# Optimization experiments

Measured on AMD Instinct MI355X. Metric: run time of the kernel, lower is better.

The kernel has to match this reference:

```python
import jax, jax.numpy as jnp
import numpy as np

N_NODES, N_EDGES, CH, FEAT = 20000, 320000, 256, 118


def setup_inputs() -> dict:
    key = jax.random.key(0)
    ks = jax.random.split(key, 8)
    x = jax.random.uniform(ks[0], (N_NODES, FEAT), dtype=jnp.float32)
    edge_index = jax.random.randint(ks[1], (2, N_EDGES), 0, N_NODES, dtype=jnp.int64)
    s = 0.05
    W_embed = jax.random.normal(ks[2], (FEAT, CH), dtype=jnp.float32) * s
    b_embed = jnp.zeros((CH,), jnp.float32)
    W1 = jax.random.normal(ks[3], (CH, CH), dtype=jnp.float32) * s
    b1 = jnp.zeros((CH,), jnp.float32)
    W2 = jax.random.normal(ks[4], (CH, CH), dtype=jnp.float32) * s
    b2 = jnp.zeros((CH,), jnp.float32)
    return {"x": x, "edge_index": edge_index, "W_embed": W_embed, "b_embed": b_embed,
            "W1": W1, "b1": b1, "W2": W2, "b2": b2}


def reference(x, edge_index, W_embed, b_embed, W1, b1, W2, b2):
    n = x.shape[0]
    # node embedding: Linear(118 -> C)
    h = x @ W_embed + b_embed  # [N, C]
    src, dst = edge_index[0], edge_index[1]
    # message: gather x_j per edge, dense1 + exact GELU (dropout = identity in eval)
    msg = jax.nn.gelu(h[src] @ W1 + b1, approximate=False)  # [E, C]
    # mean aggregation into destination nodes
    agg = jax.ops.segment_sum(msg, dst, num_segments=n)  # [N, C]
    cnt = jax.ops.segment_sum(jnp.ones((msg.shape[0],), msg.dtype), dst, num_segments=n)
    agg = agg / jnp.maximum(cnt, 1.0)[:, None]
    # update: dense2 + exact GELU
    out = jax.nn.gelu(agg @ W2 + b2, approximate=False)  # [N, C]
    # final mean over channel dim
    return out.mean(axis=1)  # [N]
```

## Files before the change

kernel.cpp:

```cpp
#include <hip/hip_runtime.h>
#include <math.h>

#define N_NODES 20000
#define N_EDGES 320000
#define CH      256
#define FEAT    118
#define CAP     48

typedef float    f32x4 __attribute__((ext_vector_type(4)));
typedef short    s16x8 __attribute__((ext_vector_type(8)));
typedef _Float16 f16x4 __attribute__((ext_vector_type(4)));
typedef unsigned short u16;

union Frag { s16x8 v; u16 u[8]; };

__device__ __forceinline__ float gelu_exact(float x) {
    return 0.5f * x * (1.0f + erff(x * 0.70710678118654752f));
}
__device__ __forceinline__ u16 f2bf(float f) {
    unsigned u = __float_as_uint(f);
    u = (u + 0x7FFFu + ((u >> 16) & 1u)) >> 16;
    return (u16)u;
}
__device__ __forceinline__ float bf2f(u16 h) { return __uint_as_float(((unsigned)h) << 16); }

__global__ __launch_bounds__(256) void prep(const float* __restrict__ x,
                                            const int* __restrict__ ei,
                                            const float* __restrict__ We,
                                            const float* __restrict__ be,
                                            const float* __restrict__ W1,
                                            const float* __restrict__ b1,
                                            const float* __restrict__ W2,
                                            u16* __restrict__ xh, u16* __restrict__ xl,
                                            int* __restrict__ cnt, int* __restrict__ bins,
                                            u16* __restrict__ w2h, u16* __restrict__ w2l,
                                            u16* __restrict__ wch, u16* __restrict__ wcl,
                                            float* __restrict__ bc) {
    const int b = blockIdx.x, tid = threadIdx.x;
    if (b < 1250) {
        int fid = b * 256 + tid;
        int lane = fid & 63, ks = (fid >> 6) & 3, mt = fid >> 8;
        int row = mt * 16 + (lane & 15);
        int k0 = ks * 32 + (lane >> 4) * 8;
        Frag hi, lo;
        #pragma unroll
        for (int j = 0; j < 8; j++) {
            int k = k0 + j;
            float v = (k < FEAT) ? x[(size_t)row * FEAT + k] : 0.0f;
            u16 h = f2bf(v);
            hi.u[j] = h; lo.u[j] = f2bf(v - bf2f(h));
        }
        ((s16x8*)xh)[fid] = hi.v;
        ((s16x8*)xl)[fid] = lo.v;
    } else if (b < 2500) {
        int e = (b - 1250) * 256 + tid;
        int s = ei[e];
        int d = ei[N_EDGES + e];
        int p = atomicAdd(&cnt[d], 1);
        if (p < CAP) bins[(size_t)d * CAP + p] = s;
    } else if (b < 2532) {
        int fid = (b - 2500) * 256 + tid;
        int lane = fid & 63, ks = (fid >> 6) & 7, nt = fid >> 9;
        int n = nt * 16 + (lane & 15);
        int k0 = ks * 32 + (lane >> 4) * 8;
        Frag hi, lo;
        #pragma unroll
        for (int j = 0; j < 8; j++) {
            float v = W2[(size_t)(k0 + j) * 256 + n];
            u16 h = f2bf(v);
            hi.u[j] = h; lo.u[j] = f2bf(v - bf2f(h));
        }
        ((s16x8*)w2h)[fid] = hi.v;
        ((s16x8*)w2l)[fid] = lo.v;
    } else {
        int f = b - 2532;
        int n = tid;
        if (f < 128) {
            float acc = 0.0f;
            if (f < FEAT) {
                const float* wr = We + (size_t)f * 256;
                #pragma unroll 8
                for (int c = 0; c < 256; c++) acc += wr[c] * W1[(size_t)c * 256 + n];
            }
            int nt = n >> 4, lm = n & 15, ks = f >> 5, q = (f >> 3) & 3, j = f & 7;
            size_t idx = (((size_t)nt * 4 + ks) * 64 + q * 16 + lm) * 8 + j;
            u16 h = f2bf(acc);
            wch[idx] = h;
            wcl[idx] = f2bf(acc - bf2f(h));
        } else {
            float acc = b1[n];
            #pragma unroll 8
            for (int c = 0; c < 256; c++) acc += be[c] * W1[(size_t)c * 256 + n];
            bc[n] = acc;
        }
    }
}

__global__ __launch_bounds__(256) void gemm_main(const u16* __restrict__ Ah_, const u16* __restrict__ Al_,
                                                 const u16* __restrict__ Bh_, const u16* __restrict__ Bl_,
                                                 const float* __restrict__ bias,
                                                 _Float16* __restrict__ Mout) {
    __shared__ _Float16 Ls[32][256];
    const int tid = threadIdx.x, wave = tid >> 6, lane = tid & 63;
    const int quad = lane >> 4, lm = lane & 15;
    const int mt0 = blockIdx.x * 2, nt0 = wave * 4;
    const s16x8* Ah = (const s16x8*)Ah_; const s16x8* Al = (const s16x8*)Al_;
    const s16x8* Bh = (const s16x8*)Bh_; const s16x8* Bl = (const s16x8*)Bl_;
    f32x4 acc[2][4];
    #pragma unroll
    for (int mi = 0; mi < 2; mi++)
        #pragma unroll
        for (int t = 0; t < 4; t++) acc[mi][t] = f32x4{0.f, 0.f, 0.f, 0.f};
    #pragma unroll
    for (int ks = 0; ks < 4; ks++) {
        s16x8 a0h = Ah[((size_t)(mt0 + 0) * 4 + ks) * 64 + lane];
        s16x8 a0l = Al[((size_t)(mt0 + 0) * 4 + ks) * 64 + lane];
        s16x8 a1h = Ah[((size_t)(mt0 + 1) * 4 + ks) * 64 + lane];
        s16x8 a1l = Al[((size_t)(mt0 + 1) * 4 + ks) * 64 + lane];
        #pragma unroll
        for (int t = 0; t < 4; t++) {
            s16x8 bh = Bh[((size_t)(nt0 + t) * 4 + ks) * 64 + lane];
            s16x8 bl = Bl[((size_t)(nt0 + t) * 4 + ks) * 64 + lane];
            acc[0][t] = __builtin_amdgcn_mfma_f32_16x16x32_bf16(a0h, bh, acc[0][t], 0, 0, 0);
            acc[0][t] = __builtin_amdgcn_mfma_f32_16x16x32_bf16(a0l, bh, acc[0][t], 0, 0, 0);
            acc[0][t] = __builtin_amdgcn_mfma_f32_16x16x32_bf16(a0h, bl, acc[0][t], 0, 0, 0);
            acc[1][t] = __builtin_amdgcn_mfma_f32_16x16x32_bf16(a1h, bh, acc[1][t], 0, 0, 0);
            acc[1][t] = __builtin_amdgcn_mfma_f32_16x16x32_bf16(a1l, bh, acc[1][t], 0, 0, 0);
            acc[1][t] = __builtin_amdgcn_mfma_f32_16x16x32_bf16(a1h, bl, acc[1][t], 0, 0, 0);
        }
    }
    #pragma unroll
    for (int t = 0; t < 4; t++) {
        float bn = bias[(nt0 + t) * 16 + lm];
        #pragma unroll
        for (int mi = 0; mi < 2; mi++)
            #pragma unroll
            for (int r = 0; r < 4; r++)
                Ls[mi * 16 + quad * 4 + r][(nt0 + t) * 16 + lm] =
                    (_Float16)gelu_exact(acc[mi][t][r] + bn);
    }
    __syncthreads();
    s16x8* dst = (s16x8*)Mout + (size_t)blockIdx.x * 1024;
    const s16x8* src = (const s16x8*)&Ls[0][0];
    #pragma unroll
    for (int it = 0; it < 4; it++)
        dst[it * 256 + tid] = src[it * 256 + tid];
}

#define LP 272
__global__ __launch_bounds__(256) void agg_mean(const _Float16* __restrict__ M,
                                                const int* __restrict__ cnt,
                                                const int* __restrict__ bins,
                                                const u16* __restrict__ Bh_, const u16* __restrict__ Bl_,
                                                const float* __restrict__ bias,
                                                float* __restrict__ out) {
    __shared__ u16 Lh[32][LP];
    __shared__ u16 Ll[32][LP];
    __shared__ float part[4][32];
    const int tid = threadIdx.x, wave = tid >> 6, lane = tid & 63;
    const int quad = lane >> 4, lm = lane & 15;

    {
        int nb = blockIdx.x * 32 + wave * 8;
        int cfull[8], cc[8], myid[8];
        #pragma unroll
        for (int i = 0; i < 8; i++) {
            cfull[i] = cnt[nb + i];
            cc[i] = min(cfull[i], CAP);
            myid[i] = (lane < CAP) ? bins[(size_t)(nb + i) * CAP + lane] : 0;
        }
        float acc[8][4];
        #pragma unroll
        for (int i = 0; i < 8; i++)
            #pragma unroll
            for (int q = 0; q < 4; q++) acc[i][q] = 0.0f;
        int mx = 0;
        #pragma unroll
        for (int i = 0; i < 8; i++) mx = max(mx, cc[i]);
        for (int j = 0; j < mx; j++) {
            #pragma unroll
            for (int i = 0; i < 8; i++) {
                if (j < cc[i]) {
                    int s = __shfl(myid[i], j, 64);
                    f16x4 v = *(const f16x4*)(M + (size_t)s * CH + lane * 4);
                    acc[i][0] += (float)v.x; acc[i][1] += (float)v.y;
                    acc[i][2] += (float)v.z; acc[i][3] += (float)v.w;
                }
            }
        }
        #pragma unroll
        for (int i = 0; i < 8; i++) {
            float inv = 1.0f / (float)max(cfull[i], 1);
            int row = wave * 8 + i;
            ushort4 hv, lv;
            u16* hp = (u16*)&hv; u16* lp = (u16*)&lv;
            #pragma unroll
            for (int q = 0; q < 4; q++) {
                float v = acc[i][q] * inv;
                u16 h = f2bf(v);
                hp[q] = h; lp[q] = f2bf(v - bf2f(h));
            }
            *(ushort4*)&Lh[row][lane * 4] = hv;
            *(ushort4*)&Ll[row][lane * 4] = lv;
        }
    }
    __syncthreads();

    const int nt0 = wave * 4;
    const s16x8* Bh = (const s16x8*)Bh_; const s16x8* Bl = (const s16x8*)Bl_;
    f32x4 acc2[2][4];
    #pragma unroll
    for (int mi = 0; mi < 2; mi++)
        #pragma unroll
        for (int t = 0; t < 4; t++) acc2[mi][t] = f32x4{0.f, 0.f, 0.f, 0.f};
    #pragma unroll
    for (int ks = 0; ks < 8; ks++) {
        int c0 = ks * 32 + quad * 8;
        s16x8 a0h = *(const s16x8*)&Lh[lm][c0];
        s16x8 a0l = *(const s16x8*)&Ll[lm][c0];
        s16x8 a1h = *(const s16x8*)&Lh[16 + lm][c0];
        s16x8 a1l = *(const s16x8*)&Ll[16 + lm][c0];
        #pragma unroll
        for (int t = 0; t < 4; t++) {
            s16x8 bh = Bh[((size_t)(nt0 + t) * 8 + ks) * 64 + lane];
            s16x8 bl = Bl[((size_t)(nt0 + t) * 8 + ks) * 64 + lane];
            acc2[0][t] = __builtin_amdgcn_mfma_f32_16x16x32_bf16(a0h, bh, acc2[0][t], 0, 0, 0);
            acc2[0][t] = __builtin_amdgcn_mfma_f32_16x16x32_bf16(a0l, bh, acc2[0][t], 0, 0, 0);
            acc2[0][t] = __builtin_amdgcn_mfma_f32_16x16x32_bf16(a0h, bl, acc2[0][t], 0, 0, 0);
            acc2[1][t] = __builtin_amdgcn_mfma_f32_16x16x32_bf16(a1h, bh, acc2[1][t], 0, 0, 0);
            acc2[1][t] = __builtin_amdgcn_mfma_f32_16x16x32_bf16(a1l, bh, acc2[1][t], 0, 0, 0);
            acc2[1][t] = __builtin_amdgcn_mfma_f32_16x16x32_bf16(a1h, bl, acc2[1][t], 0, 0, 0);
        }
    }
    float p[2][4] = {{0.f,0.f,0.f,0.f},{0.f,0.f,0.f,0.f}};
    #pragma unroll
    for (int t = 0; t < 4; t++) {
        float bn = bias[(nt0 + t) * 16 + lm];
        #pragma unroll
        for (int mi = 0; mi < 2; mi++)
            #pragma unroll
            for (int r = 0; r < 4; r++)
                p[mi][r] += gelu_exact(acc2[mi][t][r] + bn);
    }
    #pragma unroll
    for (int off = 1; off < 16; off <<= 1)
        #pragma unroll
        for (int mi = 0; mi < 2; mi++)
            #pragma unroll
            for (int r = 0; r < 4; r++)
                p[mi][r] += __shfl_xor(p[mi][r], off, 64);
    if (lm == 0)
        #pragma unroll
        for (int mi = 0; mi < 2; mi++)
            #pragma unroll
            for (int r = 0; r < 4; r++)
                part[wave][mi * 16 + quad * 4 + r] = p[mi][r];
    __syncthreads();
    if (tid < 32) {
        float s = part[0][tid] + part[1][tid] + part[2][tid] + part[3][tid];
        out[blockIdx.x * 32 + tid] = s * (1.0f / 256.0f);
    }
}

extern "C" void kernel_launch(void* const* d_in, const int* in_sizes, int n_in,
                              void* d_out, int out_size, void* d_ws, size_t ws_size,
                              hipStream_t stream) {
    const float* x  = (const float*)d_in[0];
    const int*   ei = (const int*)d_in[1];
    const float* We = (const float*)d_in[2];
    const float* be = (const float*)d_in[3];
    const float* W1 = (const float*)d_in[4];
    const float* b1 = (const float*)d_in[5];
    const float* W2 = (const float*)d_in[6];
    const float* b2 = (const float*)d_in[7];
    float* out = (float*)d_out;

    char* ws = (char*)d_ws;
    size_t off = 0;
    u16* xh = (u16*)(ws + off); off += 5120000;
    u16* xl = (u16*)(ws + off); off += 5120000;
    _Float16* M = (_Float16*)(ws + off); off += 10240000;
    u16* wch = (u16*)(ws + off); off += 65536;
    u16* wcl = (u16*)(ws + off); off += 65536;
    u16* w2h = (u16*)(ws + off); off += 131072;
    u16* w2l = (u16*)(ws + off); off += 131072;
    float* bc = (float*)(ws + off); off += 1024;
    int* cnt  = (int*)(ws + off); off += N_NODES * 4;
    int* bins = (int*)(ws + off); off += (size_t)N_NODES * CAP * 4;

    hipMemsetAsync(cnt, 0, N_NODES * sizeof(int), stream);
    prep<<<2661, 256, 0, stream>>>(x, ei, We, be, W1, b1, W2,
                                   xh, xl, cnt, bins, w2h, w2l, wch, wcl, bc);
    gemm_main<<<N_NODES / 32, 256, 0, stream>>>(xh, xl, wch, wcl, bc, M);
    agg_mean<<<N_NODES / 32, 256, 0, stream>>>(M, cnt, bins, w2h, w2l, b2, out);
}
```

Measured before the change: 178.3 us.

## Split aggregation and second GEMM into separate kernels with one wave per node

The fused gather-and-GEMM kernel becomes two kernels. The first assigns one wave per destination node and unrolls the neighbour gather four ways, which removes the per-wave max-count divergence across 8 nodes and raises parallelism. It writes the bf16 hi/lo split directly in MFMA fragment layout to global workspace. The second kernel reads those fragments for the GEMM and the GELU-mean reduction, which costs an extra global round trip and one more kernel launch.

```diff
diff --git a/kernel.cpp b/kernel.cpp
--- a/kernel.cpp
+++ b/kernel.cpp
@@ -147,89 +147,86 @@
         dst[it * 256 + tid] = src[it * 256 + tid];
 }
 
-#define LP 272
-__global__ __launch_bounds__(256) void agg_mean(const _Float16* __restrict__ M,
-                                                const int* __restrict__ cnt,
-                                                const int* __restrict__ bins,
-                                                const u16* __restrict__ Bh_, const u16* __restrict__ Bl_,
-                                                const float* __restrict__ bias,
-                                                float* __restrict__ out) {
-    __shared__ u16 Lh[32][LP];
-    __shared__ u16 Ll[32][LP];
+__global__ __launch_bounds__(256) void aggregate(const _Float16* __restrict__ M,
+                                                 const int* __restrict__ cnt,
+                                                 const int* __restrict__ bins,
+                                                 u16* __restrict__ Ah, u16* __restrict__ Al) {
+    int node = (blockIdx.x * 256 + threadIdx.x) >> 6;
+    int lane = threadIdx.x & 63;
+    int c = cnt[node];
+    int cc = min(c, CAP);
+    int myid = (lane < CAP) ? bins[(size_t)node * CAP + lane] : 0;
+    float acc[4][4];
+    #pragma unroll
+    for (int u = 0; u < 4; u++)
+        #pragma unroll
+        for (int q = 0; q < 4; q++) acc[u][q] = 0.0f;
+    int j = 0;
+    for (; j + 4 <= cc; j += 4) {
+        #pragma unroll
+        for (int u = 0; u < 4; u++) {
+            int s = __shfl(myid, j + u, 64);
+            f16x4 v = *(const f16x4*)(M + (size_t)s * CH + lane * 4);
+            acc[u][0] += (float)v.x; acc[u][1] += (float)v.y;
+            acc[u][2] += (float)v.z; acc[u][3] += (float)v.w;
+        }
+    }
+    for (; j < cc; j++) {
+        int s = __shfl(myid, j, 64);
+        f16x4 v = *(const f16x4*)(M + (size_t)s * CH + lane * 4);
+        acc[0][0] += (float)v.x; acc[0][1] += (float)v.y;
+        acc[0][2] += (float)v.z; acc[0][3] += (float)v.w;
+    }
+    float inv = 1.0f / (float)max(c, 1);
+    float vv[4];
+    #pragma unroll
+    for (int q = 0; q < 4; q++)
+        vv[q] = (acc[0][q] + acc[1][q] + acc[2][q] + acc[3][q]) * inv;
+    int mt = node >> 4, lm = node & 15;
+    int ks = lane >> 3, quad = (lane & 7) >> 1, j0 = (lane & 1) * 4;
+    size_t base = (((size_t)mt * 8 + ks) * 64 + quad * 16 + lm) * 8 + j0;
+    ushort4 hv, lv;
+    u16* hp = (u16*)&hv; u16* lp = (u16*)&lv;
+    #pragma unroll
+    for (int q = 0; q < 4; q++) {
+        u16 h = f2bf(vv[q]);
+        hp[q] = h; lp[q] = f2bf(vv[q] - bf2f(h));
+    }
+    *(ushort4*)(Ah + base) = hv;
+    *(ushort4*)(Al + base) = lv;
+}
+
+__global__ __launch_bounds__(256) void gemm_mean(const u16* __restrict__ Ah_, const u16* __restrict__ Al_,
+                                                 const u16* __restrict__ Bh_, const u16* __restrict__ Bl_,
+                                                 const float* __restrict__ bias,
+                                                 float* __restrict__ out) {
     __shared__ float part[4][32];
     const int tid = threadIdx.x, wave = tid >> 6, lane = tid & 63;
     const int quad = lane >> 4, lm = lane & 15;
-
-    {
-        int nb = blockIdx.x * 32 + wave * 8;
-        int cfull[8], cc[8], myid[8];
-        #pragma unroll
-        for (int i = 0; i < 8; i++) {
-            cfull[i] = cnt[nb + i];
-            cc[i] = min(cfull[i], CAP);
-            myid[i] = (lane < CAP) ? bins[(size_t)(nb + i) * CAP + lane] : 0;
-        }
-        float acc[8][4];
-        #pragma unroll
-        for (int i = 0; i < 8; i++)
-            #pragma unroll
-            for (int q = 0; q < 4; q++) acc[i][q] = 0.0f;
-        int mx = 0;
-        #pragma unroll
-        for (int i = 0; i < 8; i++) mx = max(mx, cc[i]);
-        for (int j = 0; j < mx; j++) {
-            #pragma unroll
-            for (int i = 0; i < 8; i++) {
-                if (j < cc[i]) {
-                    int s = __shfl(myid[i], j, 64);
-                    f16x4 v = *(const f16x4*)(M + (size_t)s * CH + lane * 4);
-                    acc[i][0] += (float)v.x; acc[i][1] += (float)v.y;
-                    acc[i][2] += (float)v.z; acc[i][3] += (float)v.w;
-                }
-            }
-        }
-        #pragma unroll
-        for (int i = 0; i < 8; i++) {
-            float inv = 1.0f / (float)max(cfull[i], 1);
-            int row = wave * 8 + i;
-            ushort4 hv, lv;
-            u16* hp = (u16*)&hv; u16* lp = (u16*)&lv;
-            #pragma unroll
-            for (int q = 0; q < 4; q++) {
-                float v = acc[i][q] * inv;
-                u16 h = f2bf(v);
-                hp[q] = h; lp[q] = f2bf(v - bf2f(h));
-            }
-            *(ushort4*)&Lh[row][lane * 4] = hv;
-            *(ushort4*)&Ll[row][lane * 4] = lv;
-        }
-    }
-    __syncthreads();
-
-    const int nt0 = wave * 4;
+    const int mt0 = blockIdx.x * 2, nt0 = wave * 4;
+    const s16x8* Ah = (const s16x8*)Ah_; const s16x8* Al = (const s16x8*)Al_;
     const s16x8* Bh = (const s16x8*)Bh_; const s16x8* Bl = (const s16x8*)Bl_;
-    f32x4 acc2[2][4];
+    f32x4 acc[2][4];
     #pragma unroll
     for (int mi = 0; mi < 2; mi++)
         #pragma unroll
-        for (int t = 0; t < 4; t++) acc2[mi][t] = f32x4{0.f, 0.f, 0.f, 0.f};
+        for (int t = 0; t < 4; t++) acc[mi][t] = f32x4{0.f, 0.f, 0.f, 0.f};
     #pragma unroll
     for (int ks = 0; ks < 8; ks++) {
-        int c0 = ks * 32 + quad * 8;
-        s16x8 a0h = *(const s16x8*)&Lh[lm][c0];
-        s16x8 a0l = *(const s16x8*)&Ll[lm][c0];
-        s16x8 a1h = *(const s16x8*)&Lh[16 + lm][c0];
-        s16x8 a1l = *(const s16x8*)&Ll[16 + lm][c0];
+        s16x8 a0h = Ah[((size_t)(mt0 + 0) * 8 + ks) * 64 + lane];
+        s16x8 a0l = Al[((size_t)(mt0 + 0) * 8 + ks) * 64 + lane];
+        s16x8 a1h = Ah[((size_t)(mt0 + 1) * 8 + ks) * 64 + lane];
+        s16x8 a1l = Al[((size_t)(mt0 + 1) * 8 + ks) * 64 + lane];
         #pragma unroll
         for (int t = 0; t < 4; t++) {
             s16x8 bh = Bh[((size_t)(nt0 + t) * 8 + ks) * 64 + lane];
             s16x8 bl = Bl[((size_t)(nt0 + t) * 8 + ks) * 64 + lane];
-            acc2[0][t] = __builtin_amdgcn_mfma_f32_16x16x32_bf16(a0h, bh, acc2[0][t], 0, 0, 0);
-            acc2[0][t] = __builtin_amdgcn_mfma_f32_16x16x32_bf16(a0l, bh, acc2[0][t], 0, 0, 0);
-            acc2[0][t] = __builtin_amdgcn_mfma_f32_16x16x32_bf16(a0h, bl, acc2[0][t], 0, 0, 0);
-            acc2[1][t] = __builtin_amdgcn_mfma_f32_16x16x32_bf16(a1h, bh, acc2[1][t], 0, 0, 0);
-            acc2[1][t] = __builtin_amdgcn_mfma_f32_16x16x32_bf16(a1l, bh, acc2[1][t], 0, 0, 0);
-            acc2[1][t] = __builtin_amdgcn_mfma_f32_16x16x32_bf16(a1h, bl, acc2[1][t], 0, 0, 0);
+            acc[0][t] = __builtin_amdgcn_mfma_f32_16x16x32_bf16(a0h, bh, acc[0][t], 0, 0, 0);
+            acc[0][t] = __builtin_amdgcn_mfma_f32_16x16x32_bf16(a0l, bh, acc[0][t], 0, 0, 0);
+            acc[0][t] = __builtin_amdgcn_mfma_f32_16x16x32_bf16(a0h, bl, acc[0][t], 0, 0, 0);
+            acc[1][t] = __builtin_amdgcn_mfma_f32_16x16x32_bf16(a1h, bh, acc[1][t], 0, 0, 0);
+            acc[1][t] = __builtin_amdgcn_mfma_f32_16x16x32_bf16(a1l, bh, acc[1][t], 0, 0, 0);
+            acc[1][t] = __builtin_amdgcn_mfma_f32_16x16x32_bf16(a1h, bl, acc[1][t], 0, 0, 0);
         }
     }
     float p[2][4] = {{0.f,0.f,0.f,0.f},{0.f,0.f,0.f,0.f}};
@@ -240,7 +237,7 @@
         for (int mi = 0; mi < 2; mi++)
             #pragma unroll
             for (int r = 0; r < 4; r++)
-                p[mi][r] += gelu_exact(acc2[mi][t][r] + bn);
+                p[mi][r] += gelu_exact(acc[mi][t][r] + bn);
     }
     #pragma unroll
     for (int off = 1; off < 16; off <<= 1)
@@ -277,9 +274,11 @@
 
     char* ws = (char*)d_ws;
     size_t off = 0;
-    u16* xh = (u16*)(ws + off); off += 5120000;
+    u16* xh = (u16*)(ws + off);
+    u16* aggh = (u16*)(ws + off); off += 5120000;
     u16* xl = (u16*)(ws + off); off += 5120000;
     _Float16* M = (_Float16*)(ws + off); off += 10240000;
+    u16* aggl = (u16*)(ws + off); off += 10240000;
     u16* wch = (u16*)(ws + off); off += 65536;
     u16* wcl = (u16*)(ws + off); off += 65536;
     u16* w2h = (u16*)(ws + off); off += 131072;
@@ -292,5 +291,6 @@
     prep<<<2661, 256, 0, stream>>>(x, ei, We, be, W1, b1, W2,
                                    xh, xl, cnt, bins, w2h, w2l, wch, wcl, bc);
     gemm_main<<<N_NODES / 32, 256, 0, stream>>>(xh, xl, wch, wcl, bc, M);
-    agg_mean<<<N_NODES / 32, 256, 0, stream>>>(M, cnt, bins, w2h, w2l, b2, out);
-}
+    aggregate<<<N_NODES / 4, 256, 0, stream>>>(M, cnt, bins, aggh, aggl);
+    gemm_mean<<<N_NODES / 32, 256, 0, stream>>>(aggh, aggl, w2h, w2l, b2, out);
+}
```

Result: faster. 155.5 us (-12.7%).
